# Optimization experiments

Hardware: AMD Instinct MI355X
Metric: run time of the kernel (lower is better)

Reference implementation:

```python
import jax, jax.numpy as jnp
import numpy as np

N_NODES = 207
N_EDGES = 1722
N_SLOTS = 288
RESOLUTION = 1
BATCH = 1024


def setup_inputs() -> dict:
    key = jax.random.key(0)
    ks = jax.random.split(key, 8)
    inputs = jax.random.normal(ks[0], (BATCH, 2, 12, N_NODES), dtype=jnp.float32)
    weight_react = jax.random.normal(ks[1], (N_SLOTS, N_EDGES), dtype=jnp.float32) / 10.0
    weight_diff = jax.random.normal(ks[2], (N_SLOTS, N_EDGES), dtype=jnp.float32) / 1000.0
    bias_reaction = jax.random.normal(ks[3], (N_SLOTS, N_NODES), dtype=jnp.float32) / 10.0
    bias_diffusion = jax.random.normal(ks[4], (N_SLOTS, N_NODES), dtype=jnp.float32) / 10.0
    weight_self_loop = jax.random.normal(ks[5], (N_SLOTS, N_NODES), dtype=jnp.float32) / 10.0
    ind = jax.random.randint(ks[6], (BATCH,), 0, N_SLOTS, dtype=jnp.int32)
    edge_index = jax.random.randint(ks[7], (2, N_EDGES), 0, N_NODES, dtype=jnp.int32)
    return {
        'inputs': inputs,
        'weight_react': weight_react,
        'weight_diff': weight_diff,
        'bias_reaction': bias_reaction,
        'bias_diffusion': bias_diffusion,
        'weight_self_loop': weight_self_loop,
        'ind': ind,
        'edge_index': edge_index,
    }


def _build_adjacency(edge_index, vals):
    """Symmetric dense adjacency per batch element.

    edge_index: [2, E] int; vals: [B, E] float.
    Returns A [B, N, N] with A[b, i, j] += v and A[b, j, i] += v (duplicates summed,
    matching torch.sparse_coo_tensor coalescing).
    """
    src = jnp.concatenate([edge_index[0], edge_index[1]])  # [2E]
    dst = jnp.concatenate([edge_index[1], edge_index[0]])  # [2E]
    v = jnp.concatenate([vals, vals], axis=1)              # [B, 2E]
    B = vals.shape[0]
    A = jnp.zeros((B, N_NODES, N_NODES), dtype=vals.dtype)
    return A.at[:, src, dst].add(v)


def reference(inputs, weight_react, weight_diff, bias_reaction, bias_diffusion,
              weight_self_loop, ind, edge_index):
    B = inputs.shape[0]
    # [B, d1, d2, N] -> [B, d1*d2, N] -> [B, N, L]
    x = inputs.reshape(B, -1, N_NODES).transpose(0, 2, 1)
    ii = ind // RESOLUTION  # time-of-day slot per sample, [B]

    A_r = _build_adjacency(edge_index, weight_react[ii])  # [B, N, N]
    A_d = _build_adjacency(edge_index, weight_diff[ii])   # [B, N, N]
    diag = jnp.arange(N_NODES)
    # torch sums dim 1 of [N, N] (column sums) and adds/subtracts diag of it
    d_r = A_r.sum(axis=1)  # [B, N]
    d_d = A_d.sum(axis=1)  # [B, N]
    R = A_r.at[:, diag, diag].add(d_r)   # diag(d) + A
    D = (-A_d).at[:, diag, diag].add(d_d)  # diag(d) - A

    # nconv: out[b, w, l] = sum_v x[b, v, l] * A[b, w, v]
    reaction = jnp.einsum('bvl,bwv->bwl', x, R) + bias_reaction[ii][:, :, None]
    diffusion = jnp.einsum('bvl,bwv->bwl', x, D) + bias_diffusion[ii][:, :, None]
    self_loop = weight_self_loop[ii][:, :, None] * x
    return jnp.tanh(reaction) + diffusion + x + self_loop  # [B, N, L]
```

## Files before the change

kernel.cpp:

```cpp
#include <hip/hip_runtime.h>

#define N_NODES 207
#define N_EDGES 1722
#define N_SLOTS 288
#define L_DIM 24
#define NPK 12
#define TOT_ENT (2 * N_EDGES)
#define THREADS 512

typedef float f32x2 __attribute__((ext_vector_type(2)));
typedef __fp16 h16x2 __attribute__((ext_vector_type(2)));

__device__ __forceinline__ unsigned pkrtz(float a, float b) {
    h16x2 h = __builtin_amdgcn_cvt_pkrtz(a, b);
    return __builtin_bit_cast(unsigned, h);
}
__device__ __forceinline__ f32x2 h2f(unsigned u) {
    h16x2 h = __builtin_bit_cast(h16x2, u);
    f32x2 r; r.x = (float)h.x; r.y = (float)h.y;
    return r;
}
__device__ __forceinline__ void fma_lo(unsigned& acc, unsigned wt, unsigned x) {
    asm("v_pk_fma_f16 %0, %1, %2, %0 op_sel:[0,0,0] op_sel_hi:[0,1,1]"
        : "+v"(acc) : "v"(wt), "v"(x));
}
__device__ __forceinline__ void fma_hi(unsigned& acc, unsigned wt, unsigned x) {
    asm("v_pk_fma_f16 %0, %1, %2, %0 op_sel:[1,0,0] op_sel_hi:[1,1,1]"
        : "+v"(acc) : "v"(wt), "v"(x));
}
__device__ __forceinline__ void addw(unsigned& sw, unsigned wt) {
    asm("v_pk_add_f16 %0, %1, %0" : "+v"(sw) : "v"(wt));
}
__device__ __forceinline__ float fast_tanhf(float x) {
    float e2 = __expf(2.0f * x);
    return 1.0f - 2.0f * __builtin_amdgcn_rcpf(e2 + 1.0f);
}

__global__ __launch_bounds__(THREADS, 4) void rdgcn_fused_kernel(
    const float* __restrict__ x_in,
    const float* __restrict__ w_react,
    const float* __restrict__ w_diff,
    const float* __restrict__ b_react,
    const float* __restrict__ b_diff,
    const float* __restrict__ w_self,
    const int* __restrict__ ind,
    const int* __restrict__ edge_index,
    float* __restrict__ out)
{
    __shared__ unsigned x_sh[2][N_NODES * NPK];
    __shared__ unsigned wt_sh[2][N_EDGES];
    __shared__ unsigned ent_sh[TOT_ENT + 4];

    const int tid  = threadIdx.x;
    const int h    = tid >> 8;
    const int htid = tid & 255;
    const int lane = tid & 63;
    const int wid  = tid >> 6;
    const int b    = blockIdx.x * 2 + h;
    const int s    = ind[b];

    float r[L_DIM];
    if (htid < N_NODES) {
        const float* xg = x_in + (size_t)b * (L_DIM * N_NODES);
        #pragma unroll
        for (int l = 0; l < L_DIM; ++l) r[l] = xg[l * N_NODES + htid];
    }

    int* cnt_s  = (int*)wt_sh;
    int* cur_s  = cnt_s + 208;
    int* off_s  = cur_s + 208;
    int* perm_s = off_s + 209;
    int* dcur_s = perm_s + 208;
    int* wsum_s = dcur_s + 64;

    if (tid < 208) cnt_s[tid] = 0;
    if (tid < 64)  dcur_s[tid] = 0;
    __syncthreads();

    int ei[4], ej[4];
    int ne = 0;
    for (int e = tid; e < N_EDGES; e += THREADS) {
        int i = edge_index[e];
        int j = edge_index[N_EDGES + e];
        ei[ne] = i; ej[ne] = j; ++ne;
        atomicAdd(&cnt_s[i], 1);
        atomicAdd(&cnt_s[j], 1);
    }
    __syncthreads();

    const int deg  = (tid < N_NODES) ? cnt_s[tid] : 0;
    const int dcap = deg > 63 ? 63 : deg;
    int xs = deg;
    if (tid < 256) {
        #pragma unroll
        for (int sft = 1; sft < 64; sft <<= 1) {
            int t = __shfl_up(xs, sft, 64);
            if (lane >= sft) xs += t;
        }
        if (lane == 63) wsum_s[wid] = xs;
    }
    if (tid < N_NODES) atomicAdd(&dcur_s[dcap], 1);
    __syncthreads();

    int base = 0;
    if (tid < 256) { for (int i = 0; i < wid; ++i) base += wsum_s[i]; }
    const int excl = base + xs - deg;
    if (tid < N_NODES) { off_s[tid] = excl; cur_s[tid] = excl; }
    if (tid == 255)    off_s[N_NODES] = base + xs;

    if (tid < 64) {
        int hg = dcur_s[63 - tid];
        int ys = hg;
        #pragma unroll
        for (int sft = 1; sft < 64; sft <<= 1) {
            int t = __shfl_up(ys, sft, 64);
            if (lane >= sft) ys += t;
        }
        __syncthreads();
        dcur_s[63 - tid] = ys - hg;
    } else {
        __syncthreads();
    }
    __syncthreads();

    if (tid < N_NODES) {
        int p = atomicAdd(&dcur_s[dcap], 1);
        perm_s[p] = tid;
    }
    for (int q = 0; q < ne; ++q) {
        const int e = tid + q * THREADS;
        int pi = atomicAdd(&cur_s[ei[q]], 1);
        ent_sh[pi] = (unsigned)ej[q] | ((unsigned)e << 16);
        int pj = atomicAdd(&cur_s[ej[q]], 1);
        ent_sh[pj] = (unsigned)ei[q] | ((unsigned)e << 16);
    }
    if (tid == 0) { ent_sh[TOT_ENT] = 0u; ent_sh[TOT_ENT + 1] = 0u; }
    __syncthreads();

    int w = 0, beg = 0, end = 0;
    if (htid < N_NODES) {
        w   = perm_s[htid];
        beg = off_s[w];
        end = off_s[w + 1];
    }
    __syncthreads();

    float br = 0.f, bd = 0.f, wsl = 0.f;
    if (htid < N_NODES) {
        br  = b_react[s * N_NODES + w];
        bd  = b_diff [s * N_NODES + w];
        wsl = w_self [s * N_NODES + w];
        unsigned p[NPK];
        #pragma unroll
        for (int i = 0; i < NPK; ++i) p[i] = pkrtz(r[2*i], r[2*i+1]);
        uint4* dst = reinterpret_cast<uint4*>(&x_sh[h][htid * NPK]);
        dst[0] = make_uint4(p[0], p[1], p[2],  p[3]);
        dst[1] = make_uint4(p[4], p[5], p[6],  p[7]);
        dst[2] = make_uint4(p[8], p[9], p[10], p[11]);
    }
    {
        const float* wrg = w_react + (size_t)s * N_EDGES;
        const float* wdg = w_diff  + (size_t)s * N_EDGES;
        for (int e = htid; e < N_EDGES; e += 256)
            wt_sh[h][e] = pkrtz(wrg[e], wdg[e]);
    }
    __syncthreads();

    if (htid >= N_NODES) return;

    unsigned accr[NPK] = {0,0,0,0,0,0,0,0,0,0,0,0};
    unsigned accd[NPK] = {0,0,0,0,0,0,0,0,0,0,0,0};
    unsigned sw = 0;

    const unsigned* wth = wt_sh[h];
    const unsigned* xsh = x_sh[h];
    unsigned en = ent_sh[beg];
    for (int k = beg; k < end; ++k) {
        const unsigned en_nx = ent_sh[k + 1];
        const int nbr = (int)(en & 0xffffu);
        const int e   = (int)(en >> 16);
        const unsigned wt = wth[e];
        const uint4* xr = reinterpret_cast<const uint4*>(&xsh[nbr * NPK]);
        const uint4 qa = xr[0], qb = xr[1], qc = xr[2];
        en = en_nx;
        addw(sw, wt);
        fma_lo(accr[0],  wt, qa.x);   fma_hi(accd[0],  wt, qa.x);
        fma_lo(accr[1],  wt, qa.y);   fma_hi(accd[1],  wt, qa.y);
        fma_lo(accr[2],  wt, qa.z);   fma_hi(accd[2],  wt, qa.z);
        fma_lo(accr[3],  wt, qa.w);   fma_hi(accd[3],  wt, qa.w);
        fma_lo(accr[4],  wt, qb.x);   fma_hi(accd[4],  wt, qb.x);
        fma_lo(accr[5],  wt, qb.y);   fma_hi(accd[5],  wt, qb.y);
        fma_lo(accr[6],  wt, qb.z);   fma_hi(accd[6],  wt, qb.z);
        fma_lo(accr[7],  wt, qb.w);   fma_hi(accd[7],  wt, qb.w);
        fma_lo(accr[8],  wt, qc.x);   fma_hi(accd[8],  wt, qc.x);
        fma_lo(accr[9],  wt, qc.y);   fma_hi(accd[9],  wt, qc.y);
        fma_lo(accr[10], wt, qc.z);   fma_hi(accd[10], wt, qc.z);
        fma_lo(accr[11], wt, qc.w);   fma_hi(accd[11], wt, qc.w);
    }

    const f32x2 sw2 = h2f(sw);
    const float swr = sw2.x, swd = sw2.y;

    const uint4* xw = reinterpret_cast<const uint4*>(&xsh[w * NPK]);
    const uint4 r0 = xw[0], r1 = xw[1], r2 = xw[2];
    const unsigned own[NPK] = { r0.x, r0.y, r0.z, r0.w,
                                r1.x, r1.y, r1.z, r1.w,
                                r2.x, r2.y, r2.z, r2.w };

    float o[L_DIM];
    #pragma unroll
    for (int i = 0; i < NPK; ++i) {
        const f32x2 xv = h2f(own[i]);
        const f32x2 ar = h2f(accr[i]);
        const f32x2 ad = h2f(accd[i]);
        {
            float re = fmaf(swr, xv.x,  ar.x) + br;
            float di = fmaf(swd, xv.x, -ad.x) + bd;
            o[2*i]   = fast_tanhf(re) + di + fmaf(xv.x, wsl, xv.x);
        }
        {
            float re = fmaf(swr, xv.y,  ar.y) + br;
            float di = fmaf(swd, xv.y, -ad.y) + bd;
            o[2*i+1] = fast_tanhf(re) + di + fmaf(xv.y, wsl, xv.y);
        }
    }
    float* op = out + (size_t)b * (N_NODES * L_DIM) + (size_t)w * L_DIM;
    reinterpret_cast<float4*>(op)[0] = make_float4(o[0],  o[1],  o[2],  o[3]);
    reinterpret_cast<float4*>(op)[1] = make_float4(o[4],  o[5],  o[6],  o[7]);
    reinterpret_cast<float4*>(op)[2] = make_float4(o[8],  o[9],  o[10], o[11]);
    reinterpret_cast<float4*>(op)[3] = make_float4(o[12], o[13], o[14], o[15]);
    reinterpret_cast<float4*>(op)[4] = make_float4(o[16], o[17], o[18], o[19]);
    reinterpret_cast<float4*>(op)[5] = make_float4(o[20], o[21], o[22], o[23]);
}

extern "C" void kernel_launch(void* const* d_in, const int* in_sizes, int n_in,
                              void* d_out, int out_size, void* d_ws, size_t ws_size,
                              hipStream_t stream) {
    const float* x_in     = (const float*)d_in[0];
    const float* w_react  = (const float*)d_in[1];
    const float* w_diff   = (const float*)d_in[2];
    const float* b_react  = (const float*)d_in[3];
    const float* b_diff   = (const float*)d_in[4];
    const float* w_self   = (const float*)d_in[5];
    const int*   ind      = (const int*)d_in[6];
    const int*   edge_idx = (const int*)d_in[7];
    float* out = (float*)d_out;

    const int B = in_sizes[6];
    rdgcn_fused_kernel<<<B / 2, THREADS, 0, stream>>>(x_in, w_react, w_diff,
                                                      b_react, b_diff, w_self,
                                                      ind, edge_idx, out);
}
```

Baseline: 25.58 us.

## Process four batch samples per block, two per thread, sharing CSR traversal

```diff
diff --git a/kernel.cpp b/kernel.cpp
--- a/kernel.cpp
+++ b/kernel.cpp
@@ -36,7 +36,7 @@
     return 1.0f - 2.0f * __builtin_amdgcn_rcpf(e2 + 1.0f);
 }
 
-__global__ __launch_bounds__(THREADS, 4) void rdgcn_fused_kernel(
+__global__ __launch_bounds__(THREADS, 2) void rdgcn_fused_kernel(
     const float* __restrict__ x_in,
     const float* __restrict__ w_react,
     const float* __restrict__ w_diff,
@@ -47,8 +47,8 @@
     const int* __restrict__ edge_index,
     float* __restrict__ out)
 {
-    __shared__ unsigned x_sh[2][N_NODES * NPK];
-    __shared__ unsigned wt_sh[2][N_EDGES];
+    __shared__ unsigned x_sh[4][N_NODES * NPK];
+    __shared__ unsigned wt_sh[4][N_EDGES];
     __shared__ unsigned ent_sh[TOT_ENT + 4];
 
     const int tid  = threadIdx.x;
@@ -56,17 +56,23 @@
     const int htid = tid & 255;
     const int lane = tid & 63;
     const int wid  = tid >> 6;
-    const int b    = blockIdx.x * 2 + h;
-    const int s    = ind[b];
-
-    float r[L_DIM];
+    const int bA   = blockIdx.x * 4 + 2 * h;
+    const int bB   = bA + 1;
+    const int sA   = ind[bA];
+    const int sB   = ind[bB];
+
+    float rA[L_DIM], rB[L_DIM];
     if (htid < N_NODES) {
-        const float* xg = x_in + (size_t)b * (L_DIM * N_NODES);
-        #pragma unroll
-        for (int l = 0; l < L_DIM; ++l) r[l] = xg[l * N_NODES + htid];
-    }
-
-    int* cnt_s  = (int*)wt_sh;
+        const float* xgA = x_in + (size_t)bA * (L_DIM * N_NODES);
+        const float* xgB = x_in + (size_t)bB * (L_DIM * N_NODES);
+        #pragma unroll
+        for (int l = 0; l < L_DIM; ++l) {
+            rA[l] = xgA[l * N_NODES + htid];
+            rB[l] = xgB[l * N_NODES + htid];
+        }
+    }
+
+    int* cnt_s  = (int*)x_sh;
     int* cur_s  = cnt_s + 208;
     int* off_s  = cur_s + 208;
     int* perm_s = off_s + 209;
@@ -145,92 +151,137 @@
     }
     __syncthreads();
 
-    float br = 0.f, bd = 0.f, wsl = 0.f;
+    float brA = 0.f, bdA = 0.f, wslA = 0.f;
+    float brB = 0.f, bdB = 0.f, wslB = 0.f;
     if (htid < N_NODES) {
-        br  = b_react[s * N_NODES + w];
-        bd  = b_diff [s * N_NODES + w];
-        wsl = w_self [s * N_NODES + w];
-        unsigned p[NPK];
-        #pragma unroll
-        for (int i = 0; i < NPK; ++i) p[i] = pkrtz(r[2*i], r[2*i+1]);
-        uint4* dst = reinterpret_cast<uint4*>(&x_sh[h][htid * NPK]);
-        dst[0] = make_uint4(p[0], p[1], p[2],  p[3]);
-        dst[1] = make_uint4(p[4], p[5], p[6],  p[7]);
-        dst[2] = make_uint4(p[8], p[9], p[10], p[11]);
+        brA  = b_react[sA * N_NODES + w];
+        bdA  = b_diff [sA * N_NODES + w];
+        wslA = w_self [sA * N_NODES + w];
+        brB  = b_react[sB * N_NODES + w];
+        bdB  = b_diff [sB * N_NODES + w];
+        wslB = w_self [sB * N_NODES + w];
+        unsigned pA[NPK], pB[NPK];
+        #pragma unroll
+        for (int i = 0; i < NPK; ++i) {
+            pA[i] = pkrtz(rA[2*i], rA[2*i+1]);
+            pB[i] = pkrtz(rB[2*i], rB[2*i+1]);
+        }
+        uint4* dA = reinterpret_cast<uint4*>(&x_sh[2*h][htid * NPK]);
+        dA[0] = make_uint4(pA[0], pA[1], pA[2],  pA[3]);
+        dA[1] = make_uint4(pA[4], pA[5], pA[6],  pA[7]);
+        dA[2] = make_uint4(pA[8], pA[9], pA[10], pA[11]);
+        uint4* dB = reinterpret_cast<uint4*>(&x_sh[2*h+1][htid * NPK]);
+        dB[0] = make_uint4(pB[0], pB[1], pB[2],  pB[3]);
+        dB[1] = make_uint4(pB[4], pB[5], pB[6],  pB[7]);
+        dB[2] = make_uint4(pB[8], pB[9], pB[10], pB[11]);
     }
     {
-        const float* wrg = w_react + (size_t)s * N_EDGES;
-        const float* wdg = w_diff  + (size_t)s * N_EDGES;
-        for (int e = htid; e < N_EDGES; e += 256)
-            wt_sh[h][e] = pkrtz(wrg[e], wdg[e]);
+        const float* wrgA = w_react + (size_t)sA * N_EDGES;
+        const float* wdgA = w_diff  + (size_t)sA * N_EDGES;
+        const float* wrgB = w_react + (size_t)sB * N_EDGES;
+        const float* wdgB = w_diff  + (size_t)sB * N_EDGES;
+        for (int e = htid; e < N_EDGES; e += 256) {
+            wt_sh[2*h][e]   = pkrtz(wrgA[e], wdgA[e]);
+            wt_sh[2*h+1][e] = pkrtz(wrgB[e], wdgB[e]);
+        }
     }
     __syncthreads();
 
     if (htid >= N_NODES) return;
 
-    unsigned accr[NPK] = {0,0,0,0,0,0,0,0,0,0,0,0};
-    unsigned accd[NPK] = {0,0,0,0,0,0,0,0,0,0,0,0};
-    unsigned sw = 0;
-
-    const unsigned* wth = wt_sh[h];
-    const unsigned* xsh = x_sh[h];
+    unsigned accrA[NPK] = {0,0,0,0,0,0,0,0,0,0,0,0};
+    unsigned accdA[NPK] = {0,0,0,0,0,0,0,0,0,0,0,0};
+    unsigned accrB[NPK] = {0,0,0,0,0,0,0,0,0,0,0,0};
+    unsigned accdB[NPK] = {0,0,0,0,0,0,0,0,0,0,0,0};
+    unsigned swA = 0, swB = 0;
+
+    const unsigned* wtA = wt_sh[2*h];
+    const unsigned* wtB = wt_sh[2*h+1];
+    const unsigned* xA  = x_sh[2*h];
+    const unsigned* xB  = x_sh[2*h+1];
     unsigned en = ent_sh[beg];
     for (int k = beg; k < end; ++k) {
         const unsigned en_nx = ent_sh[k + 1];
         const int nbr = (int)(en & 0xffffu);
         const int e   = (int)(en >> 16);
-        const unsigned wt = wth[e];
-        const uint4* xr = reinterpret_cast<const uint4*>(&xsh[nbr * NPK]);
-        const uint4 qa = xr[0], qb = xr[1], qc = xr[2];
+        const unsigned wa = wtA[e];
+        const unsigned wb = wtB[e];
+        const uint4* xra = reinterpret_cast<const uint4*>(&xA[nbr * NPK]);
+        const uint4 qa0 = xra[0], qa1 = xra[1], qa2 = xra[2];
+        const uint4* xrb = reinterpret_cast<const uint4*>(&xB[nbr * NPK]);
+        const uint4 qb0 = xrb[0], qb1 = xrb[1], qb2 = xrb[2];
         en = en_nx;
-        addw(sw, wt);
-        fma_lo(accr[0],  wt, qa.x);   fma_hi(accd[0],  wt, qa.x);
-        fma_lo(accr[1],  wt, qa.y);   fma_hi(accd[1],  wt, qa.y);
-        fma_lo(accr[2],  wt, qa.z);   fma_hi(accd[2],  wt, qa.z);
-        fma_lo(accr[3],  wt, qa.w);   fma_hi(accd[3],  wt, qa.w);
-        fma_lo(accr[4],  wt, qb.x);   fma_hi(accd[4],  wt, qb.x);
-        fma_lo(accr[5],  wt, qb.y);   fma_hi(accd[5],  wt, qb.y);
-        fma_lo(accr[6],  wt, qb.z);   fma_hi(accd[6],  wt, qb.z);
-        fma_lo(accr[7],  wt, qb.w);   fma_hi(accd[7],  wt, qb.w);
-        fma_lo(accr[8],  wt, qc.x);   fma_hi(accd[8],  wt, qc.x);
-        fma_lo(accr[9],  wt, qc.y);   fma_hi(accd[9],  wt, qc.y);
-        fma_lo(accr[10], wt, qc.z);   fma_hi(accd[10], wt, qc.z);
-        fma_lo(accr[11], wt, qc.w);   fma_hi(accd[11], wt, qc.w);
-    }
-
-    const f32x2 sw2 = h2f(sw);
-    const float swr = sw2.x, swd = sw2.y;
-
-    const uint4* xw = reinterpret_cast<const uint4*>(&xsh[w * NPK]);
-    const uint4 r0 = xw[0], r1 = xw[1], r2 = xw[2];
-    const unsigned own[NPK] = { r0.x, r0.y, r0.z, r0.w,
-                                r1.x, r1.y, r1.z, r1.w,
-                                r2.x, r2.y, r2.z, r2.w };
-
-    float o[L_DIM];
+        addw(swA, wa);
+        addw(swB, wb);
+        fma_lo(accrA[0],  wa, qa0.x);   fma_hi(accdA[0],  wa, qa0.x);
+        fma_lo(accrA[1],  wa, qa0.y);   fma_hi(accdA[1],  wa, qa0.y);
+        fma_lo(accrA[2],  wa, qa0.z);   fma_hi(accdA[2],  wa, qa0.z);
+        fma_lo(accrA[3],  wa, qa0.w);   fma_hi(accdA[3],  wa, qa0.w);
+        fma_lo(accrA[4],  wa, qa1.x);   fma_hi(accdA[4],  wa, qa1.x);
+        fma_lo(accrA[5],  wa, qa1.y);   fma_hi(accdA[5],  wa, qa1.y);
+        fma_lo(accrA[6],  wa, qa1.z);   fma_hi(accdA[6],  wa, qa1.z);
+        fma_lo(accrA[7],  wa, qa1.w);   fma_hi(accdA[7],  wa, qa1.w);
+        fma_lo(accrA[8],  wa, qa2.x);   fma_hi(accdA[8],  wa, qa2.x);
+        fma_lo(accrA[9],  wa, qa2.y);   fma_hi(accdA[9],  wa, qa2.y);
+        fma_lo(accrA[10], wa, qa2.z);   fma_hi(accdA[10], wa, qa2.z);
+        fma_lo(accrA[11], wa, qa2.w);   fma_hi(accdA[11], wa, qa2.w);
+        fma_lo(accrB[0],  wb, qb0.x);   fma_hi(accdB[0],  wb, qb0.x);
+        fma_lo(accrB[1],  wb, qb0.y);   fma_hi(accdB[1],  wb, qb0.y);
+        fma_lo(accrB[2],  wb, qb0.z);   fma_hi(accdB[2],  wb, qb0.z);
+        fma_lo(accrB[3],  wb, qb0.w);   fma_hi(accdB[3],  wb, qb0.w);
+        fma_lo(accrB[4],  wb, qb1.x);   fma_hi(accdB[4],  wb, qb1.x);
+        fma_lo(accrB[5],  wb, qb1.y);   fma_hi(accdB[5],  wb, qb1.y);
+        fma_lo(accrB[6],  wb, qb1.z);   fma_hi(accdB[6],  wb, qb1.z);
+        fma_lo(accrB[7],  wb, qb1.w);   fma_hi(accdB[7],  wb, qb1.w);
+        fma_lo(accrB[8],  wb, qb2.x);   fma_hi(accdB[8],  wb, qb2.x);
+        fma_lo(accrB[9],  wb, qb2.y);   fma_hi(accdB[9],  wb, qb2.y);
+        fma_lo(accrB[10], wb, qb2.z);   fma_hi(accdB[10], wb, qb2.z);
+        fma_lo(accrB[11], wb, qb2.w);   fma_hi(accdB[11], wb, qb2.w);
+    }
+
     #pragma unroll
-    for (int i = 0; i < NPK; ++i) {
-        const f32x2 xv = h2f(own[i]);
-        const f32x2 ar = h2f(accr[i]);
-        const f32x2 ad = h2f(accd[i]);
-        {
-            float re = fmaf(swr, xv.x,  ar.x) + br;
-            float di = fmaf(swd, xv.x, -ad.x) + bd;
-            o[2*i]   = fast_tanhf(re) + di + fmaf(xv.x, wsl, xv.x);
-        }
-        {
-            float re = fmaf(swr, xv.y,  ar.y) + br;
-            float di = fmaf(swd, xv.y, -ad.y) + bd;
-            o[2*i+1] = fast_tanhf(re) + di + fmaf(xv.y, wsl, xv.y);
-        }
-    }
-    float* op = out + (size_t)b * (N_NODES * L_DIM) + (size_t)w * L_DIM;
-    reinterpret_cast<float4*>(op)[0] = make_float4(o[0],  o[1],  o[2],  o[3]);
-    reinterpret_cast<float4*>(op)[1] = make_float4(o[4],  o[5],  o[6],  o[7]);
-    reinterpret_cast<float4*>(op)[2] = make_float4(o[8],  o[9],  o[10], o[11]);
-    reinterpret_cast<float4*>(op)[3] = make_float4(o[12], o[13], o[14], o[15]);
-    reinterpret_cast<float4*>(op)[4] = make_float4(o[16], o[17], o[18], o[19]);
-    reinterpret_cast<float4*>(op)[5] = make_float4(o[20], o[21], o[22], o[23]);
+    for (int smp = 0; smp < 2; ++smp) {
+        const unsigned* xs_ = smp ? xB : xA;
+        const unsigned* accr = smp ? accrB : accrA;
+        const unsigned* accd = smp ? accdB : accdA;
+        const unsigned sw    = smp ? swB : swA;
+        const float br  = smp ? brB  : brA;
+        const float bd  = smp ? bdB  : bdA;
+        const float wsl = smp ? wslB : wslA;
+        const int   bo  = smp ? bB   : bA;
+
+        const f32x2 sw2 = h2f(sw);
+        const float swr = sw2.x, swd = sw2.y;
+        const uint4* xw = reinterpret_cast<const uint4*>(&xs_[w * NPK]);
+        const uint4 r0 = xw[0], r1 = xw[1], r2 = xw[2];
+        const unsigned own[NPK] = { r0.x, r0.y, r0.z, r0.w,
+                                    r1.x, r1.y, r1.z, r1.w,
+                                    r2.x, r2.y, r2.z, r2.w };
+        float o[L_DIM];
+        #pragma unroll
+        for (int i = 0; i < NPK; ++i) {
+            const f32x2 xv = h2f(own[i]);
+            const f32x2 ar = h2f(accr[i]);
+            const f32x2 ad = h2f(accd[i]);
+            {
+                float re = fmaf(swr, xv.x,  ar.x) + br;
+                float di = fmaf(swd, xv.x, -ad.x) + bd;
+                o[2*i]   = fast_tanhf(re) + di + fmaf(xv.x, wsl, xv.x);
+            }
+            {
+                float re = fmaf(swr, xv.y,  ar.y) + br;
+                float di = fmaf(swd, xv.y, -ad.y) + bd;
+                o[2*i+1] = fast_tanhf(re) + di + fmaf(xv.y, wsl, xv.y);
+            }
+        }
+        float* op = out + (size_t)bo * (N_NODES * L_DIM) + (size_t)w * L_DIM;
+        reinterpret_cast<float4*>(op)[0] = make_float4(o[0],  o[1],  o[2],  o[3]);
+        reinterpret_cast<float4*>(op)[1] = make_float4(o[4],  o[5],  o[6],  o[7]);
+        reinterpret_cast<float4*>(op)[2] = make_float4(o[8],  o[9],  o[10], o[11]);
+        reinterpret_cast<float4*>(op)[3] = make_float4(o[12], o[13], o[14], o[15]);
+        reinterpret_cast<float4*>(op)[4] = make_float4(o[16], o[17], o[18], o[19]);
+        reinterpret_cast<float4*>(op)[5] = make_float4(o[20], o[21], o[22], o[23]);
+    }
 }
 
 extern "C" void kernel_launch(void* const* d_in, const int* in_sizes, int n_in,
@@ -247,7 +298,7 @@
     float* out = (float*)d_out;
 
     const int B = in_sizes[6];
-    rdgcn_fused_kernel<<<B / 2, THREADS, 0, stream>>>(x_in, w_react, w_diff,
+    rdgcn_fused_kernel<<<B / 4, THREADS, 0, stream>>>(x_in, w_react, w_diff,
                                                       b_react, b_diff, w_self,
                                                       ind, edge_idx, out);
 }
```

New measurement: 26.88 us. 1.05x slower.

## Store per-sample edge weights inline with CSR entries to remove indirect lookup

Applied to the files above, without the earlier changes.

```diff
diff --git a/kernel.cpp b/kernel.cpp
--- a/kernel.cpp
+++ b/kernel.cpp
@@ -48,16 +48,18 @@
     float* __restrict__ out)
 {
     __shared__ unsigned x_sh[2][N_NODES * NPK];
-    __shared__ unsigned wt_sh[2][N_EDGES];
-    __shared__ unsigned ent_sh[TOT_ENT + 4];
+    __shared__ uint2    ewt_sh[2][TOT_ENT];
 
     const int tid  = threadIdx.x;
     const int h    = tid >> 8;
     const int htid = tid & 255;
     const int lane = tid & 63;
     const int wid  = tid >> 6;
-    const int b    = blockIdx.x * 2 + h;
-    const int s    = ind[b];
+    const int bA   = blockIdx.x * 2;
+    const int b    = bA + h;
+    const int sA   = ind[bA];
+    const int sB   = ind[bA + 1];
+    const int s    = h ? sB : sA;
 
     float r[L_DIM];
     if (htid < N_NODES) {
@@ -66,7 +68,7 @@
         for (int l = 0; l < L_DIM; ++l) r[l] = xg[l * N_NODES + htid];
     }
 
-    int* cnt_s  = (int*)wt_sh;
+    int* cnt_s  = (int*)x_sh;
     int* cur_s  = cnt_s + 208;
     int* off_s  = cur_s + 208;
     int* perm_s = off_s + 209;
@@ -127,14 +129,24 @@
         int p = atomicAdd(&dcur_s[dcap], 1);
         perm_s[p] = tid;
     }
-    for (int q = 0; q < ne; ++q) {
-        const int e = tid + q * THREADS;
-        int pi = atomicAdd(&cur_s[ei[q]], 1);
-        ent_sh[pi] = (unsigned)ej[q] | ((unsigned)e << 16);
-        int pj = atomicAdd(&cur_s[ej[q]], 1);
-        ent_sh[pj] = (unsigned)ei[q] | ((unsigned)e << 16);
-    }
-    if (tid == 0) { ent_sh[TOT_ENT] = 0u; ent_sh[TOT_ENT + 1] = 0u; }
+    {
+        const float* wrgA = w_react + (size_t)sA * N_EDGES;
+        const float* wdgA = w_diff  + (size_t)sA * N_EDGES;
+        const float* wrgB = w_react + (size_t)sB * N_EDGES;
+        const float* wdgB = w_diff  + (size_t)sB * N_EDGES;
+        for (int q = 0; q < ne; ++q) {
+            const int e = tid + q * THREADS;
+            const unsigned wtA = pkrtz(wrgA[e], wdgA[e]);
+            const unsigned wtB = pkrtz(wrgB[e], wdgB[e]);
+            const int i = ei[q], j = ej[q];
+            int pi = atomicAdd(&cur_s[i], 1);
+            ewt_sh[0][pi] = make_uint2((unsigned)j, wtA);
+            ewt_sh[1][pi] = make_uint2((unsigned)j, wtB);
+            int pj = atomicAdd(&cur_s[j], 1);
+            ewt_sh[0][pj] = make_uint2((unsigned)i, wtA);
+            ewt_sh[1][pj] = make_uint2((unsigned)i, wtB);
+        }
+    }
     __syncthreads();
 
     int w = 0, beg = 0, end = 0;
@@ -158,12 +170,6 @@
         dst[1] = make_uint4(p[4], p[5], p[6],  p[7]);
         dst[2] = make_uint4(p[8], p[9], p[10], p[11]);
     }
-    {
-        const float* wrg = w_react + (size_t)s * N_EDGES;
-        const float* wdg = w_diff  + (size_t)s * N_EDGES;
-        for (int e = htid; e < N_EDGES; e += 256)
-            wt_sh[h][e] = pkrtz(wrg[e], wdg[e]);
-    }
     __syncthreads();
 
     if (htid >= N_NODES) return;
@@ -172,17 +178,13 @@
     unsigned accd[NPK] = {0,0,0,0,0,0,0,0,0,0,0,0};
     unsigned sw = 0;
 
-    const unsigned* wth = wt_sh[h];
+    const uint2*    ew  = ewt_sh[h];
     const unsigned* xsh = x_sh[h];
-    unsigned en = ent_sh[beg];
     for (int k = beg; k < end; ++k) {
-        const unsigned en_nx = ent_sh[k + 1];
-        const int nbr = (int)(en & 0xffffu);
-        const int e   = (int)(en >> 16);
-        const unsigned wt = wth[e];
-        const uint4* xr = reinterpret_cast<const uint4*>(&xsh[nbr * NPK]);
+        const uint2 q = ew[k];
+        const unsigned wt = q.y;
+        const uint4* xr = reinterpret_cast<const uint4*>(&xsh[q.x * NPK]);
         const uint4 qa = xr[0], qb = xr[1], qc = xr[2];
-        en = en_nx;
         addw(sw, wt);
         fma_lo(accr[0],  wt, qa.x);   fma_hi(accd[0],  wt, qa.x);
         fma_lo(accr[1],  wt, qa.y);   fma_hi(accd[1],  wt, qa.y);
```

Measured after the change: 24.51 us. 1.04x faster.
